# Kernel optimization log

Measured on AMD Instinct MI355X. Metric: run time of the kernel, lower is better.

The kernel has to match this reference:

```python
import jax, jax.numpy as jnp
import numpy as np

K = 16
N = 32
NUM_WORDS = 2 ** K  # 65536


def build_codebook(G):
    """Faithful translation of MinDistanceDecoder.init_codebook.

    Returns (possible_words [2^k, k], possible_codewords [2^k, n],
             possible_codewords_llrs [2^k, n]) in float32.
    """
    Gf = G.astype(jnp.float32)
    # coefs = round(2 ** linspace(1, k, k)) = [2, 4, ..., 2^k]
    coefs = jnp.round(2.0 ** jnp.linspace(1.0, float(K), K))  # [k]
    # linspace(0, 2^k-1, 2^k) hits exact integers; floor is identity here
    idx = jnp.floor(jnp.linspace(0.0, float(NUM_WORDS) - 1.0, NUM_WORDS))  # [2^k]
    pw = idx[:, None] % coefs[None, :]  # [2^k, k]
    sub = jnp.concatenate([jnp.zeros((NUM_WORDS, 1), jnp.float32), pw[:, :-1]], axis=-1)
    possible_words = (pw - sub) / (coefs / 2.0)  # binary bits, LSB-first
    possible_codewords = (possible_words @ Gf) % 2.0  # [2^k, n]
    possible_codewords_llrs = -1.0 * (possible_codewords * 2.0 - 1.0)  # +/-1 BPSK LLR signs
    return possible_words, possible_codewords, possible_codewords_llrs


def setup_inputs() -> dict:
    key = jax.random.key(0)
    k1, k2 = jax.random.split(key)
    noisy_symbols = jax.random.normal(k1, (64, N), dtype=jnp.float32)
    G = jax.random.randint(k2, (K, N), 0, 2, dtype=jnp.int32)
    sigma2 = jnp.ones((1,), dtype=jnp.float32)
    return {"noisy_symbols": noisy_symbols, "G": G, "sigma2": sigma2}


def reference(noisy_symbols, G, sigma2):
    possible_words, possible_codewords, cw_llrs = build_codebook(G)
    llrs = -4.0 * noisy_symbols.astype(jnp.float32) / sigma2  # [B, n]
    max_abs = jnp.max(jnp.abs(llrs))  # global max over broadcast tensor == max over llrs
    # mean |llr - max_abs * codeword_llr| per (batch, codeword): [B, 2^k]
    dist = jnp.mean(jnp.abs(llrs[:, None, :] - max_abs * cw_llrs[None, :, :]), axis=-1)
    best = jnp.argmin(dist, axis=-1)  # [B]
    # return_words=True -> gather message words
    return possible_words[best]  # [B, k]
```

## Files before the change

### kernel.cpp

```cpp
#include <hip/hip_runtime.h>
#include <stdint.h>

#define B 64
#define N 32
#define K 16
#define NUM_WORDS 65536
#define NBLK 256
#define WPB 256
#define NTHR 512

typedef unsigned long long u64;

static __device__ __forceinline__ u64 umax64(u64 a, u64 b) { return a > b ? a : b; }

__global__ __launch_bounds__(NTHR) void mdd_corr(
    const float* __restrict__ noisy,
    const int* __restrict__ G,
    const float* __restrict__ sigma2,
    u64* __restrict__ ws)
{
    __shared__ __align__(16) uint32_t cw_lds[WPB];
    __shared__ float T_lds[4 * 64 * 64];
    __shared__ float bestf_lds[8 * 64];
    __shared__ uint32_t bestw_lds[8 * 64];

    const int tid = threadIdx.x;
    const int l = tid & 63;
    const int wv = tid >> 6;
    const int g = wv & 3;
    const int h = wv >> 2;

    const float scale = -4.0f / sigma2[0];

    if (wv < 4) {
        uint32_t grows[K];
        #pragma unroll
        for (int k = 0; k < K; k += 2) {
            int gv = G[k * N + l];
            u64 m = __ballot(gv & 1);
            grows[k] = (uint32_t)m;
            grows[k + 1] = (uint32_t)(m >> 32);
        }
        uint32_t w = blockIdx.x * WPB + tid;
        uint32_t cw = 0;
        #pragma unroll
        for (int k = 0; k < K; ++k)
            cw ^= grows[k] & (0u - ((w >> k) & 1u));
        cw_lds[tid] = cw;
    }

    {
        const float* nb = noisy + l * N + 6 * g;
        float l0 = scale * nb[0];
        float l1 = scale * nb[1];
        float l2 = scale * nb[2];
        float l3 = scale * nb[3];
        float l4 = scale * nb[4];
        float l5 = scale * nb[5];
        float l5s = h ? -l5 : l5;
        float P01[4] = { l0 + l1, -l0 + l1, l0 - l1, -l0 - l1 };
        float P23[4] = { l2 + l3, -l2 + l3, l2 - l3, -l2 - l3 };
        float Q0 = l4 + l5s, Q1 = -l4 + l5s;
        float* Tp = &T_lds[g * 4096 + h * 32 * 64 + l];
        #pragma unroll
        for (int j = 0; j < 32; ++j)
            Tp[j * 64] = (P01[j & 3] + P23[(j >> 2) & 3]) + ((j & 16) ? Q1 : Q0);
    }

    uint32_t lau[8];
    #pragma unroll
    for (int v = 0; v < 8; ++v)
        lau[v] = __float_as_uint(scale * noisy[l * N + 24 + v]);

    __syncthreads();

    const uint4* cw4 = reinterpret_cast<const uint4*>(cw_lds);
    const float* Tl = &T_lds[l];
    float bestf = -INFINITY;
    uint32_t bestw = 0;
    const uint32_t wbase = blockIdx.x * WPB + wv * 32;

    #pragma unroll
    for (int wq = 0; wq < 8; ++wq) {
        uint4 c4 = cw4[wv * 8 + wq];
        #pragma unroll
        for (int e = 0; e < 4; ++e) {
            uint32_t cw = (e == 0) ? c4.x : (e == 1) ? c4.y : (e == 2) ? c4.z : c4.w;
            float r0 = Tl[0 * 4096 + ((cw >> 0) & 63u) * 64];
            float r1 = Tl[1 * 4096 + ((cw >> 6) & 63u) * 64];
            float r2 = Tl[2 * 4096 + ((cw >> 12) & 63u) * 64];
            float r3 = Tl[3 * 4096 + ((cw >> 18) & 63u) * 64];
            float v0 = __uint_as_float(lau[0] ^ ((cw << 7) & 0x80000000u));
            float v1 = __uint_as_float(lau[1] ^ ((cw << 6) & 0x80000000u));
            float v2 = __uint_as_float(lau[2] ^ ((cw << 5) & 0x80000000u));
            float v3 = __uint_as_float(lau[3] ^ ((cw << 4) & 0x80000000u));
            float v4 = __uint_as_float(lau[4] ^ ((cw << 3) & 0x80000000u));
            float v5 = __uint_as_float(lau[5] ^ ((cw << 2) & 0x80000000u));
            float v6 = __uint_as_float(lau[6] ^ ((cw << 1) & 0x80000000u));
            float v7 = __uint_as_float(lau[7] ^ ((cw << 0) & 0x80000000u));
            float c = ((r0 + r1) + (r2 + r3))
                    + (((v0 + v1) + (v2 + v3)) + ((v4 + v5) + (v6 + v7)));
            uint32_t w = wbase + wq * 4 + e;
            bool gt = c > bestf;
            bestw = gt ? w : bestw;
            bestf = gt ? c : bestf;
        }
    }

    bestf_lds[wv * 64 + l] = bestf;
    bestw_lds[wv * 64 + l] = bestw;
    __syncthreads();

    if (tid < B) {
        float f = bestf_lds[tid];
        uint32_t w = bestw_lds[tid];
        #pragma unroll
        for (int v = 1; v < 8; ++v) {
            float f2 = bestf_lds[v * 64 + tid];
            uint32_t w2 = bestw_lds[v * 64 + tid];
            bool gt = f2 > f;
            w = gt ? w2 : w;
            f = gt ? f2 : f;
        }
        uint32_t bits = __float_as_uint(f);
        uint32_t mono = (bits & 0x80000000u) ? ~bits : (bits | 0x80000000u);
        u64 key = ((u64)mono << 16) | (u64)(0xFFFFu - w);
        ws[(size_t)tid * NBLK + blockIdx.x] = key;
    }
}

__global__ __launch_bounds__(64) void mdd_out(
    const u64* __restrict__ ws,
    float* __restrict__ out)
{
    const int b = blockIdx.x;
    const int t = threadIdx.x;
    const u64* p = ws + (size_t)b * NBLK;

    u64 m = umax64(umax64(p[t], p[t + 64]), umax64(p[t + 128], p[t + 192]));
    #pragma unroll
    for (int off = 32; off > 0; off >>= 1) {
        u64 o = __shfl_xor(m, off, 64);
        m = umax64(m, o);
    }
    uint32_t w = 0xFFFFu - (uint32_t)(m & 0xFFFFull);
    if (t < K) out[b * K + t] = (float)((w >> t) & 1u);
}

extern "C" void kernel_launch(void* const* d_in, const int* in_sizes, int n_in,
                              void* d_out, int out_size, void* d_ws, size_t ws_size,
                              hipStream_t stream) {
    const float* noisy = (const float*)d_in[0];
    const int* G = (const int*)d_in[1];
    const float* sigma2 = (const float*)d_in[2];
    float* out = (float*)d_out;
    u64* ws = (u64*)d_ws;

    (void)in_sizes; (void)n_in; (void)out_size; (void)ws_size;

    mdd_corr<<<NBLK, NTHR, 0, stream>>>(noisy, G, sigma2, ws);
    mdd_out<<<B, 64, 0, stream>>>(ws, out);
}
```

Baseline: 15.21 us.

## Double block threads, stage transposed LLRs in LDS, split argmax chains

Raises the block size from 512 to 1024 threads, so each wave scores 16 codewords instead of 32 and the T-table build is split four ways per group. The noisy LLRs are first loaded coalesced into a padded transposed LDS array, replacing strided global reads. The running argmax uses two independent chains to shorten the dependency path, and the per-wave results are packed into u64 keys that are reduced with integer max. This adds a barrier and more LDS use, and caps each CU at one block.

```diff
diff --git a/kernel.cpp b/kernel.cpp
--- a/kernel.cpp
+++ b/kernel.cpp
@@ -7,7 +7,8 @@
 #define NUM_WORDS 65536
 #define NBLK 256
 #define WPB 256
-#define NTHR 512
+#define NTHR 1024
+#define LLR_PAD 65
 
 typedef unsigned long long u64;
 
@@ -21,16 +22,22 @@
 {
     __shared__ __align__(16) uint32_t cw_lds[WPB];
     __shared__ float T_lds[4 * 64 * 64];
-    __shared__ float bestf_lds[8 * 64];
-    __shared__ uint32_t bestw_lds[8 * 64];
+    __shared__ float llr_t[N * LLR_PAD];
+    __shared__ u64 bestk_lds[16 * 64];
 
     const int tid = threadIdx.x;
     const int l = tid & 63;
     const int wv = tid >> 6;
     const int g = wv & 3;
-    const int h = wv >> 2;
+    const int q = wv >> 2;
 
     const float scale = -4.0f / sigma2[0];
+
+    #pragma unroll
+    for (int i = tid; i < B * N; i += NTHR) {
+        int n = i & 31, bb = i >> 5;
+        llr_t[n * LLR_PAD + bb] = scale * noisy[i];
+    }
 
     if (wv < 4) {
         uint32_t grows[K];
@@ -48,41 +55,41 @@
             cw ^= grows[k] & (0u - ((w >> k) & 1u));
         cw_lds[tid] = cw;
     }
+    __syncthreads();
 
     {
-        const float* nb = noisy + l * N + 6 * g;
-        float l0 = scale * nb[0];
-        float l1 = scale * nb[1];
-        float l2 = scale * nb[2];
-        float l3 = scale * nb[3];
-        float l4 = scale * nb[4];
-        float l5 = scale * nb[5];
-        float l5s = h ? -l5 : l5;
+        float l0 = llr_t[(6 * g + 0) * LLR_PAD + l];
+        float l1 = llr_t[(6 * g + 1) * LLR_PAD + l];
+        float l2 = llr_t[(6 * g + 2) * LLR_PAD + l];
+        float l3 = llr_t[(6 * g + 3) * LLR_PAD + l];
+        float l4 = llr_t[(6 * g + 4) * LLR_PAD + l];
+        float l5 = llr_t[(6 * g + 5) * LLR_PAD + l];
+        float l4s = (q & 1) ? -l4 : l4;
+        float l5s = (q & 2) ? -l5 : l5;
+        float Q = l4s + l5s;
         float P01[4] = { l0 + l1, -l0 + l1, l0 - l1, -l0 - l1 };
         float P23[4] = { l2 + l3, -l2 + l3, l2 - l3, -l2 - l3 };
-        float Q0 = l4 + l5s, Q1 = -l4 + l5s;
-        float* Tp = &T_lds[g * 4096 + h * 32 * 64 + l];
+        float* Tp = &T_lds[g * 4096 + (q * 16) * 64 + l];
         #pragma unroll
-        for (int j = 0; j < 32; ++j)
-            Tp[j * 64] = (P01[j & 3] + P23[(j >> 2) & 3]) + ((j & 16) ? Q1 : Q0);
+        for (int j = 0; j < 16; ++j)
+            Tp[j * 64] = (P01[j & 3] + P23[j >> 2]) + Q;
     }
 
     uint32_t lau[8];
     #pragma unroll
     for (int v = 0; v < 8; ++v)
-        lau[v] = __float_as_uint(scale * noisy[l * N + 24 + v]);
-
+        lau[v] = __float_as_uint(llr_t[(24 + v) * LLR_PAD + l]);
     __syncthreads();
 
     const uint4* cw4 = reinterpret_cast<const uint4*>(cw_lds);
     const float* Tl = &T_lds[l];
-    float bestf = -INFINITY;
-    uint32_t bestw = 0;
-    const uint32_t wbase = blockIdx.x * WPB + wv * 32;
+    float fA = -INFINITY, fB = -INFINITY;
+    uint32_t wA = 0, wB = 0;
+    const uint32_t wbase = blockIdx.x * WPB + wv * 16;
 
     #pragma unroll
-    for (int wq = 0; wq < 8; ++wq) {
-        uint4 c4 = cw4[wv * 8 + wq];
+    for (int wq = 0; wq < 4; ++wq) {
+        uint4 c4 = cw4[wv * 4 + wq];
         #pragma unroll
         for (int e = 0; e < 4; ++e) {
             uint32_t cw = (e == 0) ? c4.x : (e == 1) ? c4.y : (e == 2) ? c4.z : c4.w;
@@ -101,31 +108,31 @@
             float c = ((r0 + r1) + (r2 + r3))
                     + (((v0 + v1) + (v2 + v3)) + ((v4 + v5) + (v6 + v7)));
             uint32_t w = wbase + wq * 4 + e;
-            bool gt = c > bestf;
-            bestw = gt ? w : bestw;
-            bestf = gt ? c : bestf;
+            if ((e & 1) == 0) {
+                bool gt = c > fA; wA = gt ? w : wA; fA = gt ? c : fA;
+            } else {
+                bool gt = c > fB; wB = gt ? w : wB; fB = gt ? c : fB;
+            }
         }
     }
 
-    bestf_lds[wv * 64 + l] = bestf;
-    bestw_lds[wv * 64 + l] = bestw;
+    {
+        uint32_t ba = __float_as_uint(fA);
+        uint32_t ma = (ba & 0x80000000u) ? ~ba : (ba | 0x80000000u);
+        uint32_t bb = __float_as_uint(fB);
+        uint32_t mb = (bb & 0x80000000u) ? ~bb : (bb | 0x80000000u);
+        u64 kA = ((u64)ma << 16) | (u64)(0xFFFFu - wA);
+        u64 kB = ((u64)mb << 16) | (u64)(0xFFFFu - wB);
+        bestk_lds[wv * 64 + l] = umax64(kA, kB);
+    }
     __syncthreads();
 
     if (tid < B) {
-        float f = bestf_lds[tid];
-        uint32_t w = bestw_lds[tid];
+        u64 m = bestk_lds[tid];
         #pragma unroll
-        for (int v = 1; v < 8; ++v) {
-            float f2 = bestf_lds[v * 64 + tid];
-            uint32_t w2 = bestw_lds[v * 64 + tid];
-            bool gt = f2 > f;
-            w = gt ? w2 : w;
-            f = gt ? f2 : f;
-        }
-        uint32_t bits = __float_as_uint(f);
-        uint32_t mono = (bits & 0x80000000u) ? ~bits : (bits | 0x80000000u);
-        u64 key = ((u64)mono << 16) | (u64)(0xFFFFu - w);
-        ws[(size_t)tid * NBLK + blockIdx.x] = key;
+        for (int v = 1; v < 16; ++v)
+            m = umax64(m, bestk_lds[v * 64 + tid]);
+        ws[(size_t)tid * NBLK + blockIdx.x] = m;
     }
 }
 
```

Measured after the change: 14.70 us. 1.03x faster.
